# Kernel optimization log

Measured on AMD Instinct MI355X. Metric: run time of the kernel, lower is better.

The kernel has to match this reference:

```python
import jax, jax.numpy as jnp
import numpy as np

DIM = 1024
HEADS = 16
DIM_HEAD = 64


def setup_inputs() -> dict:
    key = jax.random.key(0)
    k1, k2 = jax.random.split(key)
    x = jax.random.normal(k1, (2, 2048, DIM), dtype=jnp.float32)
    # to_qkv: Linear(dim, 3*heads*dim_head, bias=False); torch weight is [out,in],
    # we store the transposed [in,out] form for x @ W.
    W_qkv = jax.random.normal(k2, (DIM, 3 * HEADS * DIM_HEAD), dtype=jnp.float32) * (DIM ** -0.5)
    return {"x": x, "W_qkv": W_qkv}


def reference(x, W_qkv):
    b, n, _ = x.shape
    h, d = HEADS, DIM_HEAD
    scale = d ** -0.5
    qkv = x @ W_qkv                              # [b, n, 3*h*d]
    q, k, v = jnp.split(qkv, 3, axis=-1)
    # 'b n (h d) -> b h n d'
    q = q.reshape(b, n, h, d).transpose(0, 2, 1, 3)
    k = k.reshape(b, n, h, d).transpose(0, 2, 1, 3)
    v = v.reshape(b, n, h, d).transpose(0, 2, 1, 3)
    dots = jnp.einsum('bhnd,bhmd->bhnm', q, k) * scale
    attn = jax.nn.softmax(dots, axis=-1)
    out = jnp.einsum('bhnm,bhmd->bhnd', attn, v)
    out = out.transpose(0, 2, 1, 3).reshape(b, n, h * d)  # 'b h n d -> b n (h d)'
    return out + x  # residual (to_out is never applied in the source forward)
```

## Files before the change

### kernel.cpp

```cpp
#include <hip/hip_runtime.h>

#define DIM   1024
#define NQKV  3072
#define SEQ   2048
#define HEADS 16
#define DHEAD 64
#define M_TOT 4096

typedef __bf16 bf16;
typedef __bf16 bf16x8 __attribute__((ext_vector_type(8)));
typedef float  f32x4  __attribute__((ext_vector_type(4)));

typedef const __attribute__((address_space(1))) unsigned int gu32;
typedef __attribute__((address_space(3))) unsigned int su32;

static __device__ __forceinline__ unsigned short f2b(float f) {
    bf16 h = (bf16)f;
    return __builtin_bit_cast(unsigned short, h);
}

#define CAST_BLOCKS (M_TOT * DIM / (256 * 4))
#define TR_NB (NQKV / 64)
__global__ void prep_kernel(const float* __restrict__ x,
                            unsigned short* __restrict__ xb,
                            const float* __restrict__ W,
                            unsigned short* __restrict__ Wt) {
    __shared__ float tile[64][65];
    const int id  = blockIdx.x;
    const int tid = threadIdx.x;
    if (id < CAST_BLOCKS) {
        int i = (id * 256 + tid) * 4;
        float4 v = *(const float4*)(x + i);
        ushort4 o;
        o.x = f2b(v.x); o.y = f2b(v.y); o.z = f2b(v.z); o.w = f2b(v.w);
        *(ushort4*)(xb + i) = o;
    } else {
        int t  = id - CAST_BLOCKS;
        int nb = t % TR_NB;
        int kb = t / TR_NB;
        #pragma unroll
        for (int p = 0; p < 4; p++) {
            int kl = p * 16 + (tid >> 4);
            int nl = (tid & 15) * 4;
            float4 v = *(const float4*)&W[(size_t)(kb * 64 + kl) * NQKV + nb * 64 + nl];
            tile[nl + 0][kl] = v.x;
            tile[nl + 1][kl] = v.y;
            tile[nl + 2][kl] = v.z;
            tile[nl + 3][kl] = v.w;
        }
        __syncthreads();
        #pragma unroll
        for (int p = 0; p < 2; p++) {
            int nl = p * 32 + (tid >> 3);
            int k8 = (tid & 7) * 8;
            int n  = nb * 64 + nl;
            float s = (n < 1024) ? 0.18033688f : 1.0f;
            float4 a = *(const float4*)&tile[nl][k8];
            float4 b = *(const float4*)&tile[nl][k8 + 4];
            ushort4 o0, o1;
            o0.x = f2b(a.x * s); o0.y = f2b(a.y * s); o0.z = f2b(a.z * s); o0.w = f2b(a.w * s);
            o1.x = f2b(b.x * s); o1.y = f2b(b.y * s); o1.z = f2b(b.z * s); o1.w = f2b(b.w * s);
            uint4 pk;
            pk.x = ((unsigned)o0.y << 16) | o0.x;
            pk.y = ((unsigned)o0.w << 16) | o0.z;
            pk.z = ((unsigned)o1.y << 16) | o1.x;
            pk.w = ((unsigned)o1.w << 16) | o1.z;
            *(uint4*)&Wt[(size_t)n * DIM + kb * 64 + k8] = pk;
        }
    }
}

#define LDC 136
__global__ __launch_bounds__(256) void qkv_gemm_kernel(
    const unsigned short* __restrict__ A,
    const unsigned short* __restrict__ Bt,
    unsigned short* __restrict__ Qw,
    unsigned short* __restrict__ Kw,
    unsigned short* __restrict__ Vtw)
{
    __shared__ __align__(16) unsigned char smem[128 * LDC * 2];
    unsigned short* As = (unsigned short*)smem;
    unsigned short* Bs = (unsigned short*)(smem + 16384);
    unsigned short* Cs = (unsigned short*)smem;

    const int tid  = threadIdx.x;
    const int m0   = blockIdx.y * 128;
    const int n0   = blockIdx.x * 128;
    const int w    = tid >> 6;
    const int lane = tid & 63;
    const int l16  = lane & 15;
    const int quad = lane >> 4;
    const int wm   = (w >> 1) * 64;
    const int wn   = (w & 1) * 64;
    const int srow = lane >> 3;
    const int scol = ((lane & 7) ^ srow) * 8;
    const int xa   = l16 & 7;

    f32x4 acc[4][4];
    const f32x4 fzero = {0.f, 0.f, 0.f, 0.f};
    for (int i = 0; i < 4; i++)
        for (int j = 0; j < 4; j++) acc[i][j] = fzero;

    const unsigned short* Ag = A  + (size_t)(m0 + w * 32 + srow) * DIM + scol;
    const unsigned short* Bg = Bt + (size_t)(n0 + w * 32 + srow) * DIM + scol;

    for (int kt = 0; kt < DIM; kt += 64) {
        #pragma unroll
        for (int j = 0; j < 4; j++) {
            __builtin_amdgcn_global_load_lds((gu32*)(Ag + kt + (size_t)j * 8 * DIM),
                                             (su32*)&As[(w * 32 + j * 8) * 64], 16, 0, 0);
            __builtin_amdgcn_global_load_lds((gu32*)(Bg + kt + (size_t)j * 8 * DIM),
                                             (su32*)&Bs[(w * 32 + j * 8) * 64], 16, 0, 0);
        }
        __syncthreads();
        #pragma unroll
        for (int s = 0; s < 2; s++) {
            const int col = ((s * 4 + quad) ^ xa) * 8;
            bf16x8 af[4], bfr[4];
            #pragma unroll
            for (int i = 0; i < 4; i++) {
                af[i]  = *(const bf16x8*)(&As[(wm + i * 16 + l16) * 64 + col]);
                bfr[i] = *(const bf16x8*)(&Bs[(wn + i * 16 + l16) * 64 + col]);
            }
            #pragma unroll
            for (int i = 0; i < 4; i++)
                #pragma unroll
                for (int j = 0; j < 4; j++)
                    acc[i][j] = __builtin_amdgcn_mfma_f32_16x16x32_bf16(af[i], bfr[j], acc[i][j], 0, 0, 0);
        }
        __syncthreads();
    }

    const int part = n0 >> 10;
    const int h0   = (n0 & 1023) >> 6;
    const int b    = m0 >> 11;
    const int np0  = m0 & 2047;

    if (part < 2) {
        #pragma unroll
        for (int i = 0; i < 4; i++)
            #pragma unroll
            for (int j = 0; j < 4; j++)
                #pragma unroll
                for (int r = 0; r < 4; r++)
                    Cs[(wm + i * 16 + quad * 4 + r) * LDC + wn + j * 16 + l16] = f2b(acc[i][j][r]);
        __syncthreads();
        unsigned short* dst = (part == 0) ? Qw : Kw;
        #pragma unroll
        for (int pass = 0; pass < 8; pass++) {
            int mi = pass * 16 + (tid >> 4);
            int ci = (tid & 15) * 8;
            uint4 v = *(const uint4*)&Cs[mi * LDC + ci];
            int bh = b * HEADS + h0 + (ci >> 6);
            *(uint4*)&dst[((size_t)bh * SEQ + np0 + mi) * DHEAD + (ci & 63)] = v;
        }
    } else {
        #pragma unroll
        for (int i = 0; i < 4; i++)
            #pragma unroll
            for (int j = 0; j < 4; j++) {
                ushort4 pk;
                pk.x = f2b(acc[i][j][0]); pk.y = f2b(acc[i][j][1]);
                pk.z = f2b(acc[i][j][2]); pk.w = f2b(acc[i][j][3]);
                *(ushort4*)&Cs[(wn + j * 16 + l16) * LDC + wm + i * 16 + quad * 4] = pk;
            }
        __syncthreads();
        #pragma unroll
        for (int pass = 0; pass < 8; pass++) {
            int ci = pass * 16 + (tid >> 4);
            int mi = (tid & 15) * 8;
            uint4 v = *(const uint4*)&Cs[ci * LDC + mi];
            int bh = b * HEADS + h0 + (ci >> 6);
            *(uint4*)&Vtw[((size_t)bh * DHEAD + (ci & 63)) * SEQ + np0 + mi] = v;
        }
    }
}

#define KT 16
__global__ __launch_bounds__(512, 4) void attn_kernel(
    const unsigned short* __restrict__ Qw,
    const unsigned short* __restrict__ Kw,
    const unsigned short* __restrict__ Vtw,
    const float* __restrict__ x,
    float* __restrict__ out)
{
    __shared__ __align__(16) unsigned char smem[32768];
    unsigned short* KsU = (unsigned short*)smem;
    unsigned short* VsU = KsU + 8192;
    float* scratch = (float*)smem;

    const int id  = blockIdx.x;
    const int qt  = id >> 5;
    const int bh  = ((id & 7) << 2) | ((id >> 3) & 3);
    const int tid = threadIdx.x;
    const int w   = tid >> 6, lane = tid & 63;
    const int l16 = lane & 15, quad = lane >> 4;
    const int g   = w & 3;
    const int p   = w >> 2;
    const int xq  = l16 & 7;

    const unsigned short* Qb = Qw + ((size_t)bh * SEQ + qt * 128 + g * 32 + l16) * DHEAD;
    bf16x8 qf[2][2];
    #pragma unroll
    for (int qh = 0; qh < 2; qh++) {
        qf[qh][0] = *(const bf16x8*)(Qb + qh * 16 * DHEAD + quad * 8);
        qf[qh][1] = *(const bf16x8*)(Qb + qh * 16 * DHEAD + 32 + quad * 8);
    }

    bf16x8 ones;
    #pragma unroll
    for (int j = 0; j < 8; j++) ones[j] = (bf16)1.0f;

    f32x4 o[2][4], dsum[2];
    const f32x4 fzero = {0.f, 0.f, 0.f, 0.f};
    #pragma unroll
    for (int qh = 0; qh < 2; qh++) {
        #pragma unroll
        for (int d = 0; d < 4; d++) o[qh][d] = fzero;
        dsum[qh] = fzero;
    }

    const unsigned short* Kg = Kw  + (size_t)bh * SEQ * DHEAD;
    const unsigned short* Vg = Vtw + (size_t)bh * DHEAD * SEQ;

    const int sl   = lane >> 3;
    const int c16s = (lane & 7) ^ sl;
    const int pr   = 8 * w + sl;
    const int rlog = ((pr >> 2) & 3) * 8 + ((pr >> 4) & 1) * 4 + (pr & 3) + (pr & 32);
    const size_t koff = (size_t)rlog * DHEAD + c16s * 8;
    const size_t voff = (size_t)pr * SEQ + c16s * 8;

    for (int t = 0; t < KT; t++) {
        __syncthreads();
        const size_t kb = (size_t)(t * 64) * DHEAD;
        __builtin_amdgcn_global_load_lds((gu32*)(Kg + kb + koff),
                                         (su32*)&KsU[w * 512], 16, 0, 0);
        __builtin_amdgcn_global_load_lds((gu32*)(Kg + kb + (size_t)1024 * DHEAD + koff),
                                         (su32*)&KsU[4096 + w * 512], 16, 0, 0);
        __builtin_amdgcn_global_load_lds((gu32*)(Vg + voff + t * 64),
                                         (su32*)&VsU[w * 512], 16, 0, 0);
        __builtin_amdgcn_global_load_lds((gu32*)(Vg + voff + 1024 + t * 64),
                                         (su32*)&VsU[4096 + w * 512], 16, 0, 0);
        __syncthreads();

        const unsigned short* Kb = KsU + p * 4096;
        const unsigned short* Vb = VsU + p * 4096;

        f32x4 sacc[2][4];
        #pragma unroll
        for (int qh = 0; qh < 2; qh++)
            #pragma unroll
            for (int ki = 0; ki < 4; ki++) sacc[qh][ki] = fzero;
        #pragma unroll
        for (int s = 0; s < 2; s++) {
            const int col = ((s * 4 + quad) ^ xq) * 8;
            #pragma unroll
            for (int ki = 0; ki < 4; ki++) {
                bf16x8 kf = *(const bf16x8*)(&Kb[(ki * 16 + l16) * 64 + col]);
                sacc[0][ki] = __builtin_amdgcn_mfma_f32_16x16x32_bf16(kf, qf[0][s], sacc[0][ki], 0, 0, 0);
                sacc[1][ki] = __builtin_amdgcn_mfma_f32_16x16x32_bf16(kf, qf[1][s], sacc[1][ki], 0, 0, 0);
            }
        }

        bf16x8 pf[2][2];
        #pragma unroll
        for (int qh = 0; qh < 2; qh++)
            #pragma unroll
            for (int s = 0; s < 2; s++)
                #pragma unroll
                for (int half = 0; half < 2; half++) {
                    int ki = 2 * s + half;
                    #pragma unroll
                    for (int r = 0; r < 4; r++)
                        pf[qh][s][half * 4 + r] = (bf16)__builtin_amdgcn_exp2f(sacc[qh][ki][r]);
                }

        #pragma unroll
        for (int s = 0; s < 2; s++) {
            const int col = ((s * 4 + quad) ^ xq) * 8;
            dsum[0] = __builtin_amdgcn_mfma_f32_16x16x32_bf16(pf[0][s], ones, dsum[0], 0, 0, 0);
            dsum[1] = __builtin_amdgcn_mfma_f32_16x16x32_bf16(pf[1][s], ones, dsum[1], 0, 0, 0);
            #pragma unroll
            for (int d = 0; d < 4; d++) {
                bf16x8 vf = *(const bf16x8*)(&Vb[(d * 16 + l16) * 64 + col]);
                o[0][d] = __builtin_amdgcn_mfma_f32_16x16x32_bf16(pf[0][s], vf, o[0][d], 0, 0, 0);
                o[1][d] = __builtin_amdgcn_mfma_f32_16x16x32_bf16(pf[1][s], vf, o[1][d], 0, 0, 0);
            }
        }
    }

    __syncthreads();
    #pragma unroll
    for (int ch = 0; ch < 2; ch++) {
        if (ch) __syncthreads();
        if (p == 1) {
            float* sc = scratch + ((size_t)(g * 64 + lane)) * 20;
            #pragma unroll
            for (int di = 0; di < 4; di++)
                *(f32x4*)(sc + di * 4) = o[ch][di];
            *(f32x4*)(sc + 16) = dsum[ch];
        }
        __syncthreads();
        if (p == 0) {
            float* sc = scratch + ((size_t)(g * 64 + lane)) * 20;
            #pragma unroll
            for (int di = 0; di < 4; di++)
                o[ch][di] += *(const f32x4*)(sc + di * 4);
            dsum[ch] += *(const f32x4*)(sc + 16);
        }
    }

    if (p == 0) {
        const int b = bh >> 4, h = bh & 15;
        #pragma unroll
        for (int ch = 0; ch < 2; ch++) {
            float lr[4];
            #pragma unroll
            for (int r = 0; r < 4; r++) lr[r] = __builtin_amdgcn_rcpf(dsum[ch][r]);
            #pragma unroll
            for (int di = 0; di < 4; di++)
                #pragma unroll
                for (int r = 0; r < 4; r++) {
                    int np  = qt * 128 + g * 32 + ch * 16 + quad * 4 + r;
                    int col = h * 64 + di * 16 + l16;
                    size_t gidx = ((size_t)(b * SEQ + np)) * DIM + col;
                    out[gidx] = o[ch][di][r] * lr[r] + x[gidx];
                }
        }
    }
}

extern "C" void kernel_launch(void* const* d_in, const int* in_sizes, int n_in,
                              void* d_out, int out_size, void* d_ws, size_t ws_size,
                              hipStream_t stream) {
    const float* x  = (const float*)d_in[0];
    const float* Wq = (const float*)d_in[1];
    float* out = (float*)d_out;

    unsigned short* xb = (unsigned short*)d_ws;
    unsigned short* Wt = xb + (size_t)M_TOT * DIM;
    unsigned short* Qw = Wt + (size_t)NQKV * DIM;
    unsigned short* Kw = Qw + (size_t)32 * SEQ * DHEAD;
    unsigned short* Vt = Kw + (size_t)32 * SEQ * DHEAD;

    prep_kernel<<<CAST_BLOCKS + TR_NB * (DIM / 64), 256, 0, stream>>>(x, xb, Wq, Wt);
    qkv_gemm_kernel<<<dim3(NQKV / 128, M_TOT / 128), 256, 0, stream>>>(xb, Wt, Qw, Kw, Vt);
    attn_kernel<<<(SEQ / 128) * 32, 512, 0, stream>>>(Qw, Kw, Vt, x, out);
}
```

Before: 149.0 us.

## Double-buffer LDS tiles in QKV GEMM and attention kernels

Both the QKV GEMM and the attention kernel now use two LDS buffers. The next K-slice (or K/V tile) is prefetched with global_load_lds while MFMAs run on the current buffer, which also removes one barrier per iteration. The aim is to hide global-load latency behind compute. In exchange, shared memory per block doubles to 64 KB, which cuts the number of blocks that can be resident per CU, especially for the attention kernel declared with 4 blocks per CU.

```diff
diff --git a/kernel.cpp b/kernel.cpp
--- a/kernel.cpp
+++ b/kernel.cpp
@@ -78,9 +78,7 @@
     unsigned short* __restrict__ Kw,
     unsigned short* __restrict__ Vtw)
 {
-    __shared__ __align__(16) unsigned char smem[128 * LDC * 2];
-    unsigned short* As = (unsigned short*)smem;
-    unsigned short* Bs = (unsigned short*)(smem + 16384);
+    __shared__ __align__(16) unsigned char smem[65536];
     unsigned short* Cs = (unsigned short*)smem;
 
     const int tid  = threadIdx.x;
@@ -104,15 +102,35 @@
     const unsigned short* Ag = A  + (size_t)(m0 + w * 32 + srow) * DIM + scol;
     const unsigned short* Bg = Bt + (size_t)(n0 + w * 32 + srow) * DIM + scol;
 
-    for (int kt = 0; kt < DIM; kt += 64) {
+    {
+        unsigned short* As0 = (unsigned short*)smem;
+        unsigned short* Bs0 = (unsigned short*)(smem + 16384);
         #pragma unroll
         for (int j = 0; j < 4; j++) {
-            __builtin_amdgcn_global_load_lds((gu32*)(Ag + kt + (size_t)j * 8 * DIM),
-                                             (su32*)&As[(w * 32 + j * 8) * 64], 16, 0, 0);
-            __builtin_amdgcn_global_load_lds((gu32*)(Bg + kt + (size_t)j * 8 * DIM),
-                                             (su32*)&Bs[(w * 32 + j * 8) * 64], 16, 0, 0);
-        }
-        __syncthreads();
+            __builtin_amdgcn_global_load_lds((gu32*)(Ag + (size_t)j * 8 * DIM),
+                                             (su32*)&As0[(w * 32 + j * 8) * 64], 16, 0, 0);
+            __builtin_amdgcn_global_load_lds((gu32*)(Bg + (size_t)j * 8 * DIM),
+                                             (su32*)&Bs0[(w * 32 + j * 8) * 64], 16, 0, 0);
+        }
+    }
+    __syncthreads();
+
+    for (int ki = 0; ki < 16; ki++) {
+        const int cur = ki & 1, nxt = cur ^ 1;
+        if (ki < 15) {
+            const int kt = (ki + 1) * 64;
+            unsigned short* Asn = (unsigned short*)(smem + nxt * 32768);
+            unsigned short* Bsn = (unsigned short*)(smem + nxt * 32768 + 16384);
+            #pragma unroll
+            for (int j = 0; j < 4; j++) {
+                __builtin_amdgcn_global_load_lds((gu32*)(Ag + kt + (size_t)j * 8 * DIM),
+                                                 (su32*)&Asn[(w * 32 + j * 8) * 64], 16, 0, 0);
+                __builtin_amdgcn_global_load_lds((gu32*)(Bg + kt + (size_t)j * 8 * DIM),
+                                                 (su32*)&Bsn[(w * 32 + j * 8) * 64], 16, 0, 0);
+            }
+        }
+        const unsigned short* As = (const unsigned short*)(smem + cur * 32768);
+        const unsigned short* Bs = (const unsigned short*)(smem + cur * 32768 + 16384);
         #pragma unroll
         for (int s = 0; s < 2; s++) {
             const int col = ((s * 4 + quad) ^ xa) * 8;
@@ -184,9 +202,8 @@
     const float* __restrict__ x,
     float* __restrict__ out)
 {
-    __shared__ __align__(16) unsigned char smem[32768];
-    unsigned short* KsU = (unsigned short*)smem;
-    unsigned short* VsU = KsU + 8192;
+    __shared__ __align__(16) unsigned char smem[65536];
+    unsigned short* base = (unsigned short*)smem;
     float* scratch = (float*)smem;
 
     const int id  = blockIdx.x;
@@ -230,21 +247,31 @@
     const size_t koff = (size_t)rlog * DHEAD + c16s * 8;
     const size_t voff = (size_t)pr * SEQ + c16s * 8;
 
+    {
+        unsigned short* Kd = base + w * 512;
+        unsigned short* Vd = base + 8192 + w * 512;
+        __builtin_amdgcn_global_load_lds((gu32*)(Kg + koff),                         (su32*)Kd, 16, 0, 0);
+        __builtin_amdgcn_global_load_lds((gu32*)(Kg + (size_t)1024 * DHEAD + koff), (su32*)(Kd + 4096), 16, 0, 0);
+        __builtin_amdgcn_global_load_lds((gu32*)(Vg + voff),                         (su32*)Vd, 16, 0, 0);
+        __builtin_amdgcn_global_load_lds((gu32*)(Vg + voff + 1024),                  (su32*)(Vd + 4096), 16, 0, 0);
+    }
+    __syncthreads();
+
     for (int t = 0; t < KT; t++) {
-        __syncthreads();
-        const size_t kb = (size_t)(t * 64) * DHEAD;
-        __builtin_amdgcn_global_load_lds((gu32*)(Kg + kb + koff),
-                                         (su32*)&KsU[w * 512], 16, 0, 0);
-        __builtin_amdgcn_global_load_lds((gu32*)(Kg + kb + (size_t)1024 * DHEAD + koff),
-                                         (su32*)&KsU[4096 + w * 512], 16, 0, 0);
-        __builtin_amdgcn_global_load_lds((gu32*)(Vg + voff + t * 64),
-                                         (su32*)&VsU[w * 512], 16, 0, 0);
-        __builtin_amdgcn_global_load_lds((gu32*)(Vg + voff + 1024 + t * 64),
-                                         (su32*)&VsU[4096 + w * 512], 16, 0, 0);
-        __syncthreads();
-
-        const unsigned short* Kb = KsU + p * 4096;
-        const unsigned short* Vb = VsU + p * 4096;
+        const int cur = t & 1, nxt = cur ^ 1;
+        if (t + 1 < KT) {
+            const size_t kb = (size_t)((t + 1) * 64) * DHEAD;
+            const int kv = (t + 1) * 64;
+            unsigned short* Kd = base + nxt * 16384 + w * 512;
+            unsigned short* Vd = base + nxt * 16384 + 8192 + w * 512;
+            __builtin_amdgcn_global_load_lds((gu32*)(Kg + kb + koff),                         (su32*)Kd, 16, 0, 0);
+            __builtin_amdgcn_global_load_lds((gu32*)(Kg + kb + (size_t)1024 * DHEAD + koff), (su32*)(Kd + 4096), 16, 0, 0);
+            __builtin_amdgcn_global_load_lds((gu32*)(Vg + voff + kv),                        (su32*)Vd, 16, 0, 0);
+            __builtin_amdgcn_global_load_lds((gu32*)(Vg + voff + 1024 + kv),                 (su32*)(Vd + 4096), 16, 0, 0);
+        }
+
+        const unsigned short* Kb = base + cur * 16384 + p * 4096;
+        const unsigned short* Vb = base + cur * 16384 + 8192 + p * 4096;
 
         f32x4 sacc[2][4];
         #pragma unroll
@@ -287,9 +314,9 @@
                 o[1][d] = __builtin_amdgcn_mfma_f32_16x16x32_bf16(pf[1][s], vf, o[1][d], 0, 0, 0);
             }
         }
-    }
-
-    __syncthreads();
+        __syncthreads();
+    }
+
     #pragma unroll
     for (int ch = 0; ch < 2; ch++) {
         if (ch) __syncthreads();
```

New measurement: 147.3 us. About the same (-1.1%).
